# Optimization experiments

Measured on AMD Instinct MI355X. Metric: run time of the kernel, lower is better.

Reference implementation:

```python
import jax, jax.numpy as jnp
import numpy as np

EPS = 1e-12  # matches torch F.normalize default eps


def _l2_normalize(x):
    # F.normalize: x / max(||x||_2, eps), along last dim
    n = jnp.sqrt(jnp.sum(x * x, axis=-1, keepdims=True))
    return x / jnp.maximum(n, EPS)


def setup_inputs() -> dict:
    key = jax.random.key(0)
    k1, k2, k3, k4 = jax.random.split(key, 4)
    N, M, D = 2048, 100000, 256
    return {
        "shape_embedding": jax.random.normal(k1, (N, D), dtype=jnp.float32),
        "gallery_embedding": jax.random.normal(k2, (M, D), dtype=jnp.float32),
        "category_idx": jax.random.randint(k3, (M,), 0, 9, dtype=jnp.int64) if jax.config.jax_enable_x64 else jax.random.randint(k3, (M,), 0, 9, dtype=jnp.int32),
        "shape_idx": jax.random.randint(k4, (M,), 0, 10000, dtype=jnp.int32),
    }


def reference(shape_embedding, gallery_embedding, category_idx, shape_idx):
    # Gallery embeddings are L2-normalized once in __init__; query normalized per call.
    g = _l2_normalize(gallery_embedding)          # [M, D]
    q = _l2_normalize(shape_embedding)            # [N, D]
    scores = jnp.einsum('nd,md->nm', q, g)        # cosine similarity [N, M]
    idx = jnp.argmax(scores, axis=-1)             # top-1 retrieval [N]
    return category_idx[idx], shape_idx[idx]
```

## Files before the change

kernel.cpp:

```cpp
#include <hip/hip_runtime.h>
#include <hip/hip_fp16.h>
#include <math.h>
#include <float.h>

#define M_G 100000
#define M_PAD 100032
#define NT64 1563
#define N_Q 2048
#define DIM 256
#define NG 3126
#define GSTR 3136
#define MARGIN 0.009f

typedef _Float16 f16x8 __attribute__((ext_vector_type(8)));
typedef float f32x4 __attribute__((ext_vector_type(4)));

#define WS_GP 0
#define WS_QP 51216384
#define WS_BM 52264960

__device__ inline unsigned pack_h2(float a, float b) {
    __half ha = __float2half(a), hb = __float2half(b);
    return (unsigned)*(unsigned short*)&ha | ((unsigned)*(unsigned short*)&hb << 16);
}
__device__ inline void gload_lds16(const void* gsrc, void* ldst) {
    __builtin_amdgcn_global_load_lds(
        (const __attribute__((address_space(1))) unsigned int*)gsrc,
        (__attribute__((address_space(3))) unsigned int*)ldst, 16, 0, 0);
}

#define BAR __builtin_amdgcn_s_barrier()
#define VMCNT(n) { asm volatile("s_waitcnt vmcnt(" #n ")" ::: "memory"); \
                   __builtin_amdgcn_sched_barrier(0); }

__global__ __launch_bounds__(256) void pack_kernel(
    const float* __restrict__ g, const float* __restrict__ q,
    uint4* __restrict__ gp, uint4* __restrict__ qp)
{
    const int b = blockIdx.x;
    const int w4 = threadIdx.x >> 6, lane = threadIdx.x & 63;
    const bool isg = b < (M_PAD / 4);
    const int row = (isg ? b : b - M_PAD / 4) * 4 + w4;
    const bool real = !isg || row < M_G;
    const float* src = isg ? g + (size_t)row * DIM : q + (size_t)row * DIM;

    float inv = 0.0f;
    if (real) {
        float4 v = ((const float4*)src)[lane];
        float ss = v.x * v.x + v.y * v.y + v.z * v.z + v.w * v.w;
        #pragma unroll
        for (int o = 32; o; o >>= 1) ss += __shfl_xor(ss, o);
        inv = 1.0f / fmaxf(sqrtf(ss), 1e-12f);
    }
    if (lane < 32) {
        uint4 w = make_uint4(0u, 0u, 0u, 0u);
        if (real) {
            float4 a = ((const float4*)src)[lane * 2];
            float4 c = ((const float4*)src)[lane * 2 + 1];
            w.x = pack_h2(a.x * inv, a.y * inv);
            w.y = pack_h2(a.z * inv, a.w * inv);
            w.z = pack_h2(c.x * inv, c.y * inv);
            w.w = pack_h2(c.z * inv, c.w * inv);
        }
        const int kt = lane >> 3, gg = lane & 7;
        if (isg) {
            int mt = row >> 6, rl = row & 63;
            gp[((size_t)mt * 4 + kt) * 512 + rl * 8 + (gg ^ (rl & 7))] = w;
        } else {
            int qt = row >> 8, rl = row & 255;
            qp[((size_t)qt * 4 + kt) * 2048 + rl * 8 + (gg ^ (rl & 7))] = w;
        }
    }
}

#define STAGE32(dstbase, src) { const uint4* s_ = (src); _Pragma("unroll") \
  for (int p_ = 0; p_ < 4; ++p_) \
    gload_lds16(s_ + p_ * 512 + tid, lds + (dstbase) + (p_ * 512 + tid) * 16); }

#define READ_BP(KT, bufbase) { _Pragma("unroll") \
  for (int nj = 0; nj < 4; ++nj) { \
    const char* p_ = lds + (bufbase) + (wc * 64 + nj * 16 + r16) * 128; \
    bR[KT][0][nj] = *(const f16x8*)(p_ + sw0); \
    bR[KT][1][nj] = *(const f16x8*)(p_ + sw1); } }

__global__ __launch_bounds__(512, 2) void scoreA_kernel(
    const uint4* __restrict__ gp, const uint4* __restrict__ qp,
    unsigned short* __restrict__ bmaxH)
{
    extern __shared__ char lds[];

    const int bid = blockIdx.x;
    const int qt = bid >> 5, mc = bid & 31;
    const int nt = (mc < 27) ? 49 : 48;
    const int t0 = (mc < 27) ? mc * 49 : 1323 + (mc - 27) * 48;

    const int tid = threadIdx.x;
    const int wid = tid >> 6, lane = tid & 63;
    const int wr = wid >> 2, wc = wid & 3;
    const int r16 = lane & 15, rhi = lane >> 4;
    const int sw0 = ((rhi ^ (r16 & 7)) << 4);
    const int sw1 = (((4 + rhi) ^ (r16 & 7)) << 4);

    const uint4* qsrc = qp + (size_t)qt * 8192;

    f16x8 bR[4][2][4];
    STAGE32(0,     qsrc + 0 * 2048);
    STAGE32(32768, qsrc + 1 * 2048);
    VMCNT(4); BAR;
    READ_BP(0, 0); BAR;
    STAGE32(0, qsrc + 2 * 2048);
    VMCNT(4); BAR;
    READ_BP(1, 32768); BAR;
    STAGE32(32768, qsrc + 3 * 2048);
    VMCNT(4); BAR;
    READ_BP(2, 0); BAR;
    STAGE32(0, gp + (size_t)t0 * 2048);
    VMCNT(4); BAR;
    READ_BP(3, 32768); BAR;
    VMCNT(0); BAR;

    for (int t = 0; t < nt; ++t) {
        const int mtile = t0 + t;
        const int cur = (t & 1) << 15;
        const int nxt = cur ^ 32768;
        if (t + 1 < nt) STAGE32(nxt, gp + (size_t)(mtile + 1) * 2048);

        f32x4 acc[2][4];
        #pragma unroll
        for (int mi = 0; mi < 2; ++mi)
            #pragma unroll
            for (int nj = 0; nj < 4; ++nj) acc[mi][nj] = (f32x4){0.f, 0.f, 0.f, 0.f};

        #pragma unroll
        for (int kt = 0; kt < 4; ++kt) {
            #pragma unroll
            for (int kk = 0; kk < 2; ++kk) {
                const char* p_ = lds + cur + kt * 8192 + (wr * 32 + r16) * 128;
                const int sw = kk ? sw1 : sw0;
                f16x8 a0 = *(const f16x8*)(p_ + sw);
                f16x8 a1 = *(const f16x8*)(p_ + 2048 + sw);
                #pragma unroll
                for (int nj = 0; nj < 4; ++nj) {
                    acc[0][nj] = __builtin_amdgcn_mfma_f32_16x16x32_f16(
                        a0, bR[kt][kk][nj], acc[0][nj], 0, 0, 0);
                    acc[1][nj] = __builtin_amdgcn_mfma_f32_16x16x32_f16(
                        a1, bR[kt][kk][nj], acc[1][nj], 0, 0, 0);
                }
            }
        }

        float cm[4] = {-FLT_MAX, -FLT_MAX, -FLT_MAX, -FLT_MAX};
        #pragma unroll
        for (int mi = 0; mi < 2; ++mi)
            #pragma unroll
            for (int jj = 0; jj < 4; ++jj)
                #pragma unroll
                for (int nj = 0; nj < 4; ++nj)
                    cm[nj] = fmaxf(cm[nj], acc[mi][nj][jj]);
        #pragma unroll
        for (int nj = 0; nj < 4; ++nj) {
            float v = cm[nj];
            v = fmaxf(v, __shfl_xor(v, 16));
            v = fmaxf(v, __shfl_xor(v, 32));
            if (lane < 16) {
                int qn = qt * 256 + wc * 64 + nj * 16 + lane;
                __half h = __float2half(v);
                bmaxH[(size_t)qn * GSTR + mtile * 2 + wr] = *(unsigned short*)&h;
            }
        }
        if (t + 1 < nt) { VMCNT(4); BAR; }
    }
}

__global__ __launch_bounds__(256) void phaseB_kernel(
    const float* __restrict__ q, const float* __restrict__ g,
    const unsigned short* __restrict__ bmaxH,
    const int* __restrict__ cat, const int* __restrict__ shp,
    int* __restrict__ out)
{
    __shared__ __align__(16) float qrow[DIM];
    __shared__ int glist[NG];
    __shared__ int ng;
    __shared__ float smax[4];
    __shared__ float rbs[4];
    __shared__ int rbi[4];

    const int qi = blockIdx.x;
    const int tid = threadIdx.x;
    const int lane = tid & 63, wid = tid >> 6;
    const __half* bm = (const __half*)(bmaxH + (size_t)qi * GSTR);
    if (tid < 64)
        *(float4*)&qrow[tid * 4] = *(const float4*)(q + (size_t)qi * DIM + tid * 4);
    if (tid == 0) ng = 0;

    float m = -FLT_MAX;
    for (int gr = tid; gr < NG; gr += 256)
        m = fmaxf(m, __half2float(bm[gr]));
    #pragma unroll
    for (int o = 32; o; o >>= 1) m = fmaxf(m, __shfl_xor(m, o));
    if (lane == 0) smax[wid] = m;
    __syncthreads();
    const float thr = fmaxf(fmaxf(smax[0], smax[1]), fmaxf(smax[2], smax[3])) - MARGIN;

    for (int gr = tid; gr < NG; gr += 256)
        if (__half2float(bm[gr]) >= thr)
            glist[atomicAdd(&ng, 1)] = gr;
    __syncthreads();

    float bs = -FLT_MAX;
    int bi = 0x7fffffff;
    const int r = tid >> 3, p = tid & 7;
    const int n = ng;
    for (int i = 0; i < n; ++i) {
        int mm = glist[i] * 32 + r;
        if (mm < M_G) {
            const float* grow = g + (size_t)mm * DIM + p * 32;
            const float* qr = qrow + p * 32;
            float s = 0.f, ssq = 0.f;
            #pragma unroll
            for (int jj = 0; jj < 8; ++jj) {
                float4 gv = *(const float4*)(grow + jj * 4);
                float4 qv = *(const float4*)(qr + jj * 4);
                s += gv.x * qv.x + gv.y * qv.y + gv.z * qv.z + gv.w * qv.w;
                ssq += gv.x * gv.x + gv.y * gv.y + gv.z * gv.z + gv.w * gv.w;
            }
            s += __shfl_xor(s, 1);  s += __shfl_xor(s, 2);  s += __shfl_xor(s, 4);
            ssq += __shfl_xor(ssq, 1); ssq += __shfl_xor(ssq, 2); ssq += __shfl_xor(ssq, 4);
            s *= 1.0f / fmaxf(sqrtf(ssq), 1e-12f);
            if (p == 0 && (s > bs || (s == bs && mm < bi))) { bs = s; bi = mm; }
        }
    }
    #pragma unroll
    for (int o = 1; o < 64; o <<= 1) {
        float os = __shfl_xor(bs, o);
        int oi = __shfl_xor(bi, o);
        if (os > bs || (os == bs && oi < bi)) { bs = os; bi = oi; }
    }
    if (lane == 0) { rbs[wid] = bs; rbi[wid] = bi; }
    __syncthreads();
    if (tid == 0) {
        #pragma unroll
        for (int ww = 1; ww < 4; ++ww)
            if (rbs[ww] > bs || (rbs[ww] == bs && rbi[ww] < bi)) { bs = rbs[ww]; bi = rbi[ww]; }
        out[qi] = cat[bi];
        out[N_Q + qi] = shp[bi];
    }
}

extern "C" void kernel_launch(void* const* d_in, const int* in_sizes, int n_in,
                              void* d_out, int out_size, void* d_ws, size_t ws_size,
                              hipStream_t stream) {
    const float* q = (const float*)d_in[0];
    const float* g = (const float*)d_in[1];
    const int* cat = (const int*)d_in[2];
    const int* shp = (const int*)d_in[3];
    int* out = (int*)d_out;

    char* ws = (char*)d_ws;
    uint4* gp            = (uint4*)(ws + WS_GP);
    uint4* qp            = (uint4*)(ws + WS_QP);
    unsigned short* bmaxH = (unsigned short*)(ws + WS_BM);

    hipFuncSetAttribute((const void*)scoreA_kernel,
                        hipFuncAttributeMaxDynamicSharedMemorySize, 65536);

    pack_kernel<<<M_PAD / 4 + N_Q / 4, 256, 0, stream>>>(g, q, gp, qp);
    scoreA_kernel<<<256, 512, 65536, stream>>>(gp, qp, bmaxH);
    phaseB_kernel<<<N_Q, 256, 0, stream>>>(q, g, bmaxH, cat, shp, out);
}
```

Measured before the change: 161.1 us.

## Double gallery tile to 128 rows per step and stage all queries at once

```diff
diff --git a/kernel.cpp b/kernel.cpp
--- a/kernel.cpp
+++ b/kernel.cpp
@@ -4,11 +4,11 @@
 #include <float.h>
 
 #define M_G 100000
-#define M_PAD 100032
-#define NT64 1563
+#define M_PAD 100096
+#define NMT 782
 #define N_Q 2048
 #define DIM 256
-#define NG 3126
+#define NG 3128
 #define GSTR 3136
 #define MARGIN 0.009f
 
@@ -16,8 +16,8 @@
 typedef float f32x4 __attribute__((ext_vector_type(4)));
 
 #define WS_GP 0
-#define WS_QP 51216384
-#define WS_BM 52264960
+#define WS_QP 51249152
+#define WS_BM 52297728
 
 __device__ inline unsigned pack_h2(float a, float b) {
     __half ha = __float2half(a), hb = __float2half(b);
@@ -30,6 +30,8 @@
 }
 
 #define BAR __builtin_amdgcn_s_barrier()
+#define LGKM0 { asm volatile("s_waitcnt lgkmcnt(0)" ::: "memory"); \
+                __builtin_amdgcn_sched_barrier(0); }
 #define VMCNT(n) { asm volatile("s_waitcnt vmcnt(" #n ")" ::: "memory"); \
                    __builtin_amdgcn_sched_barrier(0); }
 
@@ -64,8 +66,8 @@
         }
         const int kt = lane >> 3, gg = lane & 7;
         if (isg) {
-            int mt = row >> 6, rl = row & 63;
-            gp[((size_t)mt * 4 + kt) * 512 + rl * 8 + (gg ^ (rl & 7))] = w;
+            int mt = row >> 7, rl = row & 127;
+            gp[((size_t)mt * 4 + kt) * 1024 + rl * 8 + (gg ^ (rl & 7))] = w;
         } else {
             int qt = row >> 8, rl = row & 255;
             qp[((size_t)qt * 4 + kt) * 2048 + rl * 8 + (gg ^ (rl & 7))] = w;
@@ -73,9 +75,13 @@
     }
 }
 
-#define STAGE32(dstbase, src) { const uint4* s_ = (src); _Pragma("unroll") \
-  for (int p_ = 0; p_ < 4; ++p_) \
+#define STAGE64(dstbase, src) { const uint4* s_ = (src); _Pragma("unroll") \
+  for (int p_ = 0; p_ < 8; ++p_) \
     gload_lds16(s_ + p_ * 512 + tid, lds + (dstbase) + (p_ * 512 + tid) * 16); }
+
+#define STAGE_QALL { _Pragma("unroll") \
+  for (int c_ = 0; c_ < 16; ++c_) \
+    gload_lds16(qsrc + c_ * 512 + tid, lds + (c_ * 512 + tid) * 16); }
 
 #define READ_BP(KT, bufbase) { _Pragma("unroll") \
   for (int nj = 0; nj < 4; ++nj) { \
@@ -91,8 +97,8 @@
 
     const int bid = blockIdx.x;
     const int qt = bid >> 5, mc = bid & 31;
-    const int nt = (mc < 27) ? 49 : 48;
-    const int t0 = (mc < 27) ? mc * 49 : 1323 + (mc - 27) * 48;
+    const int nt = (mc < 14) ? 25 : 24;
+    const int t0 = (mc < 14) ? mc * 25 : 350 + (mc - 14) * 24;
 
     const int tid = threadIdx.x;
     const int wid = tid >> 6, lane = tid & 63;
@@ -104,71 +110,73 @@
     const uint4* qsrc = qp + (size_t)qt * 8192;
 
     f16x8 bR[4][2][4];
-    STAGE32(0,     qsrc + 0 * 2048);
-    STAGE32(32768, qsrc + 1 * 2048);
-    VMCNT(4); BAR;
-    READ_BP(0, 0); BAR;
-    STAGE32(0, qsrc + 2 * 2048);
-    VMCNT(4); BAR;
-    READ_BP(1, 32768); BAR;
-    STAGE32(32768, qsrc + 3 * 2048);
-    VMCNT(4); BAR;
-    READ_BP(2, 0); BAR;
-    STAGE32(0, gp + (size_t)t0 * 2048);
-    VMCNT(4); BAR;
-    READ_BP(3, 32768); BAR;
+    STAGE_QALL;
+    VMCNT(0); BAR;
+    READ_BP(0, 0); READ_BP(1, 32768); READ_BP(2, 65536); READ_BP(3, 98304);
+    LGKM0; BAR;
+    STAGE64(0, gp + (size_t)t0 * 4096);
     VMCNT(0); BAR;
 
     for (int t = 0; t < nt; ++t) {
         const int mtile = t0 + t;
-        const int cur = (t & 1) << 15;
-        const int nxt = cur ^ 32768;
-        if (t + 1 < nt) STAGE32(nxt, gp + (size_t)(mtile + 1) * 2048);
-
-        f32x4 acc[2][4];
-        #pragma unroll
-        for (int mi = 0; mi < 2; ++mi)
-            #pragma unroll
-            for (int nj = 0; nj < 4; ++nj) acc[mi][nj] = (f32x4){0.f, 0.f, 0.f, 0.f};
+        const int cur = (t & 1) << 16;
+        const int nxt = cur ^ 65536;
+        if (t + 1 < nt) STAGE64(nxt, gp + (size_t)(mtile + 1) * 4096);
+
+        f32x4 acc[4][4];
+        #pragma unroll
+        for (int f = 0; f < 4; ++f)
+            #pragma unroll
+            for (int nj = 0; nj < 4; ++nj) acc[f][nj] = (f32x4){0.f, 0.f, 0.f, 0.f};
 
         #pragma unroll
         for (int kt = 0; kt < 4; ++kt) {
             #pragma unroll
             for (int kk = 0; kk < 2; ++kk) {
-                const char* p_ = lds + cur + kt * 8192 + (wr * 32 + r16) * 128;
+                const char* pbase = lds + cur + kt * 16384;
                 const int sw = kk ? sw1 : sw0;
-                f16x8 a0 = *(const f16x8*)(p_ + sw);
-                f16x8 a1 = *(const f16x8*)(p_ + 2048 + sw);
+                f16x8 aR[4];
                 #pragma unroll
-                for (int nj = 0; nj < 4; ++nj) {
-                    acc[0][nj] = __builtin_amdgcn_mfma_f32_16x16x32_f16(
-                        a0, bR[kt][kk][nj], acc[0][nj], 0, 0, 0);
-                    acc[1][nj] = __builtin_amdgcn_mfma_f32_16x16x32_f16(
-                        a1, bR[kt][kk][nj], acc[1][nj], 0, 0, 0);
+                for (int f = 0; f < 4; ++f) {
+                    int row = wr * 64 + f * 16 + r16;
+                    aR[f] = *(const f16x8*)(pbase + row * 128 + sw);
                 }
-            }
-        }
-
-        float cm[4] = {-FLT_MAX, -FLT_MAX, -FLT_MAX, -FLT_MAX};
-        #pragma unroll
-        for (int mi = 0; mi < 2; ++mi)
-            #pragma unroll
-            for (int jj = 0; jj < 4; ++jj)
                 #pragma unroll
-                for (int nj = 0; nj < 4; ++nj)
-                    cm[nj] = fmaxf(cm[nj], acc[mi][nj][jj]);
-        #pragma unroll
-        for (int nj = 0; nj < 4; ++nj) {
-            float v = cm[nj];
-            v = fmaxf(v, __shfl_xor(v, 16));
-            v = fmaxf(v, __shfl_xor(v, 32));
-            if (lane < 16) {
-                int qn = qt * 256 + wc * 64 + nj * 16 + lane;
-                __half h = __float2half(v);
-                bmaxH[(size_t)qn * GSTR + mtile * 2 + wr] = *(unsigned short*)&h;
-            }
-        }
-        if (t + 1 < nt) { VMCNT(4); BAR; }
+                for (int f = 0; f < 4; ++f)
+                    #pragma unroll
+                    for (int nj = 0; nj < 4; ++nj)
+                        acc[f][nj] = __builtin_amdgcn_mfma_f32_16x16x32_f16(
+                            aR[f], bR[kt][kk][nj], acc[f][nj], 0, 0, 0);
+            }
+        }
+
+        #pragma unroll
+        for (int gidx = 0; gidx < 2; ++gidx) {
+            float cm[4] = {-FLT_MAX, -FLT_MAX, -FLT_MAX, -FLT_MAX};
+            #pragma unroll
+            for (int fo = 0; fo < 2; ++fo) {
+                int f = gidx * 2 + fo;
+                #pragma unroll
+                for (int jj = 0; jj < 4; ++jj)
+                    #pragma unroll
+                    for (int nj = 0; nj < 4; ++nj)
+                        cm[nj] = fmaxf(cm[nj], acc[f][nj][jj]);
+            }
+            const int group = mtile * 4 + wr * 2 + gidx;
+            const bool padgrp = (mtile * 128 + (wr * 2 + gidx) * 32) >= M_G;
+            #pragma unroll
+            for (int nj = 0; nj < 4; ++nj) {
+                float v = cm[nj];
+                v = fmaxf(v, __shfl_xor(v, 16));
+                v = fmaxf(v, __shfl_xor(v, 32));
+                if (lane < 16) {
+                    int qn = qt * 256 + wc * 64 + nj * 16 + lane;
+                    __half h = __float2half(padgrp ? -65504.f : v);
+                    bmaxH[(size_t)qn * GSTR + group] = *(unsigned short*)&h;
+                }
+            }
+        }
+        if (t + 1 < nt) { VMCNT(8); BAR; }
     }
 }
 
@@ -257,14 +265,14 @@
     int* out = (int*)d_out;
 
     char* ws = (char*)d_ws;
-    uint4* gp            = (uint4*)(ws + WS_GP);
-    uint4* qp            = (uint4*)(ws + WS_QP);
+    uint4* gp             = (uint4*)(ws + WS_GP);
+    uint4* qp             = (uint4*)(ws + WS_QP);
     unsigned short* bmaxH = (unsigned short*)(ws + WS_BM);
 
     hipFuncSetAttribute((const void*)scoreA_kernel,
-                        hipFuncAttributeMaxDynamicSharedMemorySize, 65536);
+                        hipFuncAttributeMaxDynamicSharedMemorySize, 131072);
 
     pack_kernel<<<M_PAD / 4 + N_Q / 4, 256, 0, stream>>>(g, q, gp, qp);
-    scoreA_kernel<<<256, 512, 65536, stream>>>(gp, qp, bmaxH);
+    scoreA_kernel<<<256, 512, 131072, stream>>>(gp, qp, bmaxH);
     phaseB_kernel<<<N_Q, 256, 0, stream>>>(q, g, bmaxH, cat, shp, out);
 }
```

New measurement: 168.2 us. +4.4%, slower.
